# Performance work log

Measured on AMD Instinct MI355X. Metric: run time of the kernel, lower is better.

Reference implementation:

```python
import jax, jax.numpy as jnp
import numpy as np

A = 5          # angRes
C = 128        # channels
SPA = 2 * C    # spa_dim
NH = 8         # num_heads
KW = 11        # mask_field[1]


def setup_inputs() -> dict:
    key = jax.random.key(0)
    ks = jax.random.split(key, 12)
    s = 0.05
    return {
        "buffer": jax.random.normal(ks[0], (2, C, A * A, 32, 32), jnp.float32),
        "Win": jax.random.normal(ks[1], (SPA, C), jnp.float32) * s,
        "ln_w": jnp.ones((SPA,), jnp.float32),
        "ln_b": jnp.zeros((SPA,), jnp.float32),
        "in_proj": jax.random.normal(ks[2], (3 * SPA, SPA), jnp.float32) * s,
        "attn_out_w": jax.random.normal(ks[3], (SPA, SPA), jnp.float32) * s,
        "ffn_ln_w": jnp.ones((SPA,), jnp.float32),
        "ffn_ln_b": jnp.zeros((SPA,), jnp.float32),
        "ff1": jax.random.normal(ks[4], (2 * SPA, SPA), jnp.float32) * s,
        "ff2": jax.random.normal(ks[5], (SPA, 2 * SPA), jnp.float32) * s,
        "Wout": jax.random.normal(ks[6], (C, SPA), jnp.float32) * s,
        "conv_w": jax.random.normal(ks[7], (C, C, 1, 3, 3), jnp.float32) * s,
    }


def layer_norm(x, w, b, eps=1e-5):
    mu = x.mean(-1, keepdims=True)
    var = ((x - mu) ** 2).mean(-1, keepdims=True)
    return (x - mu) * jax.lax.rsqrt(var + eps) * w + b


def gen_mask(h, w, k_h, k_w):
    # additive mask over flattened (h*w) x (h*w) grid, local window k_h x k_w
    i = jnp.arange(h)
    j = jnp.arange(w)
    mh = (i[None, :] >= i[:, None] - k_h // 2) & (i[None, :] < i[:, None] + (k_h - k_h // 2))
    mw = (j[None, :] >= j[:, None] - k_w // 2) & (j[None, :] < j[:, None] + (k_w - k_w // 2))
    allowed = (mh[:, None, :, None] & mw[None, :, None, :]).reshape(h * w, h * w)
    return jnp.where(allowed, 0.0, -jnp.inf)


def basic_trans(x, Win, ln_w, ln_b, in_proj, attn_out_w,
                ffn_ln_w, ffn_ln_b, ff1, ff2, Wout):
    b, c, n, v, w = x.shape
    mask = gen_mask(v, w, 2 * A, KW)                       # (L, L)
    # 'b c n v w -> (v w) (b n) c'
    tok = x.transpose(3, 4, 0, 2, 1).reshape(v * w, b * n, c)
    tok = tok @ Win.T                                       # (L, B, E)
    tn = layer_norm(tok, ln_w, ln_b)
    L, B, E = tok.shape
    hd = E // NH
    Wq, Wk, Wv = jnp.split(in_proj, 3, axis=0)
    q = (tn @ Wq.T).reshape(L, B, NH, hd)
    k = (tn @ Wk.T).reshape(L, B, NH, hd)
    vv = (tok @ Wv.T).reshape(L, B, NH, hd)                 # value = un-normed tok
    scores = jnp.einsum('lbhd,mbhd->bhlm', q, k) / np.float32(np.sqrt(hd))
    scores = scores + mask[None, None]
    attn = jax.nn.softmax(scores, axis=-1)
    o = jnp.einsum('bhlm,mbhd->lbhd', attn, vv).reshape(L, B, E)
    tok = o @ attn_out_w.T + tok
    ff = layer_norm(tok, ffn_ln_w, ffn_ln_b)
    ff = jax.nn.relu(ff @ ff1.T) @ ff2.T
    tok = ff + tok
    tok = tok @ Wout.T                                      # (L, B, c)
    # '(v w) (b n) c -> b c n v w'
    return tok.reshape(v, w, b, n, c).transpose(2, 4, 3, 0, 1)


def reference(buffer, Win, ln_w, ln_b, in_proj, attn_out_w,
              ffn_ln_w, ffn_ln_b, ff1, ff2, Wout, conv_w):
    a = A
    b, c, uv, h, w = buffer.shape
    bt = lambda z: basic_trans(z, Win, ln_w, ln_b, in_proj, attn_out_w,
                               ffn_ln_w, ffn_ln_b, ff1, ff2, Wout)
    conv = lambda z: jax.lax.conv_general_dilated(
        z, conv_w, (1, 1, 1), ((0, 0), (1, 1), (1, 1)),
        dimension_numbers=('NCDHW', 'OIDHW', 'NCDHW'))

    # pass 1: 'b c (u v) h w -> b c (v w) u h'
    x = buffer.reshape(b, c, a, a, h, w).transpose(0, 1, 3, 5, 2, 4).reshape(b, c, a * w, a, h)
    x = bt(x)
    x = x.reshape(b, c, a, w, a, h).transpose(0, 1, 4, 2, 5, 3).reshape(b, c, a * a, h, w)
    x = conv(x) + buffer
    sc2 = x
    # pass 2: 'b c (u v) h w -> b c (u h) v w'
    y = x.reshape(b, c, a, a, h, w).transpose(0, 1, 2, 4, 3, 5).reshape(b, c, a * h, a, w)
    y = bt(y)
    y = y.reshape(b, c, a, h, a, w).transpose(0, 1, 2, 4, 3, 5).reshape(b, c, a * a, h, w)
    return conv(y) + sc2
```

## Files before the change

kernel.cpp:

```cpp
#include <hip/hip_runtime.h>
#include <math.h>
#include <stdint.h>

typedef __attribute__((ext_vector_type(8))) short bf16x8;
typedef __attribute__((ext_vector_type(4))) float f32x4;

static __device__ __forceinline__ unsigned short f2bf(float f) {
    unsigned u = __builtin_bit_cast(unsigned, f);
    unsigned r = u + 0x7fffu + ((u >> 16) & 1u);
    return (unsigned short)(r >> 16);
}
static __device__ __forceinline__ float bf2f(unsigned short h) {
    return __builtin_bit_cast(float, ((unsigned)h) << 16);
}
static __device__ __forceinline__ void gload_lds16(const void* g, void* l) {
    __builtin_amdgcn_global_load_lds((const __attribute__((address_space(1))) unsigned int*)g,
                                     (__attribute__((address_space(3))) unsigned int*)l, 16, 0, 0);
}

__global__ __launch_bounds__(256) void gather1(const float* __restrict__ src,
                                               unsigned short* __restrict__ x0, int W, int bb0) {
    int cct = blockIdx.x & 3, y = blockIdx.x >> 2;
    int n = blockIdx.y; int u = n / 5, v = n % 5;
    int lb = blockIdx.z, bb = bb0 + lb;
    __shared__ float tile[32][33];
    int tx = threadIdx.x & 31, tg = threadIdx.x >> 5;
    const float* s = src + (((size_t)(bb * 128 + cct * 32) * 25 + n) * 32 + y) * 32;
    #pragma unroll
    for (int i = 0; i < 4; i++) {
        int cl = tg + 8 * i;
        tile[cl][tx] = s[(size_t)cl * 25600 + tx];
    }
    __syncthreads();
    unsigned short* d = x0 + ((size_t)(u * 32 + y) * W + lb * 160 + v * 32) * 128 + cct * 32;
    #pragma unroll
    for (int i = 0; i < 4; i++) {
        int xx = tg + 8 * i;
        d[(size_t)xx * 128 + tx] = f2bf(tile[tx][xx]);
    }
}

__global__ __launch_bounds__(256) void gather2(const float* __restrict__ src,
                                               unsigned short* __restrict__ x0, int W, int bb0) {
    int cct = blockIdx.x & 3, x = blockIdx.x >> 2;
    int n = blockIdx.y; int u = n / 5, v = n % 5;
    int lb = blockIdx.z, bb = bb0 + lb;
    __shared__ float tile[32][33];
    int tx = threadIdx.x & 31, tg = threadIdx.x >> 5;
    const float* s = src + (((size_t)(bb * 128 + cct * 32) * 25 + n) * 32) * 32 + x;
    #pragma unroll
    for (int i = 0; i < 4; i++) {
        int cl = tg + 8 * i;
        tile[cl][tx] = s[(size_t)cl * 25600 + tx * 32];
    }
    __syncthreads();
    unsigned short* d = x0 + ((size_t)(v * 32 + x) * W + lb * 160 + u * 32) * 128 + cct * 32;
    #pragma unroll
    for (int i = 0; i < 4; i++) {
        int yy = tg + 8 * i;
        d[(size_t)yy * 128 + tx] = f2bf(tile[tx][yy]);
    }
}

__global__ __launch_bounds__(256) void repack_w(const float* __restrict__ cw,
                                                unsigned short* __restrict__ wb) {
    int g = blockIdx.x * 256 + threadIdx.x;
    int co = g / 1152;
    int rem = g - co * 1152;
    int ci = rem / 9, tap = rem - ci * 9;
    wb[((size_t)tap * 128 + co) * 128 + ci] = f2bf(cw[g]);
}

__global__ __launch_bounds__(256) void conv_weights(const float* __restrict__ Win,
                                                    const float* __restrict__ in_proj,
                                                    const float* __restrict__ attn_out_w,
                                                    const float* __restrict__ ff1,
                                                    const float* __restrict__ ff2,
                                                    const float* __restrict__ Wout,
                                                    unsigned short* __restrict__ wg) {
    int g = blockIdx.x * 256 + threadIdx.x;
    float v;
    if      (g < 32768)  v = Win[g];
    else if (g < 229376) v = in_proj[g - 32768];
    else if (g < 294912) v = attn_out_w[g - 229376];
    else if (g < 425984) v = ff1[g - 294912];
    else if (g < 557056) v = ff2[g - 425984];
    else                 v = Wout[g - 557056];
    wg[g] = f2bf(v);
}

__global__ __launch_bounds__(256) void ln_bf16(const unsigned short* __restrict__ in,
                                               unsigned short* __restrict__ out,
                                               const float* __restrict__ w, const float* __restrict__ b) {
    int tok = blockIdx.x * 4 + (threadIdx.x >> 6);
    int lane = threadIdx.x & 63;
    ushort4 h4 = ((const ushort4*)(in + (size_t)tok * 256))[lane];
    float vx = bf2f(h4.x), vy = bf2f(h4.y), vz = bf2f(h4.z), vw = bf2f(h4.w);
    float s = vx + vy + vz + vw;
    #pragma unroll
    for (int off = 32; off > 0; off >>= 1) s += __shfl_xor(s, off);
    float mu = s * (1.0f / 256.0f);
    float dx = vx - mu, dy = vy - mu, dz = vz - mu, dw = vw - mu;
    float vs = dx * dx + dy * dy + dz * dz + dw * dw;
    #pragma unroll
    for (int off = 32; off > 0; off >>= 1) vs += __shfl_xor(vs, off);
    float inv = rsqrtf(vs * (1.0f / 256.0f) + 1e-5f);
    float4 wv = ((const float4*)w)[lane];
    float4 bv = ((const float4*)b)[lane];
    ushort4 o4;
    o4.x = f2bf(dx * inv * wv.x + bv.x);
    o4.y = f2bf(dy * inv * wv.y + bv.y);
    o4.z = f2bf(dz * inv * wv.z + bv.z);
    o4.w = f2bf(dw * inv * wv.w + bv.w);
    *(ushort4*)(out + (size_t)tok * 256 + lane * 4) = o4;
}

static __device__ __forceinline__ void xcd_remap(int& bxi, int& byi) {
    int d = blockIdx.x + gridDim.x * blockIdx.y;
    int s = d & 7;
    unsigned j = (unsigned)(d >> 3);
    unsigned ny = gridDim.y;
    int gm8 = (int)(gridDim.x >> 3);
    bxi = s * gm8 + (int)(j / ny);
    byi = (int)(j % ny);
}

static __device__ __forceinline__ void gemm_core64(const unsigned short* __restrict__ X,
                                                   const unsigned short* __restrict__ Wt,
                                                   int bm, int bnrow, int K,
                                                   unsigned short (&As)[2][64 * 32],
                                                   unsigned short (&Bs)[2][64 * 32],
                                                   f32x4 (&acc)[2][2]) {
    const int tid = threadIdx.x;
    const int lane = tid & 63, w = tid >> 6;
    const int wm = (w >> 1) * 32, wn = (w & 1) * 32;
    const int lr = lane & 15, lq = lane >> 4;
    #pragma unroll
    for (int m = 0; m < 2; m++)
        #pragma unroll
        for (int n = 0; n < 2; n++)
            acc[m][n] = (f32x4){0.f, 0.f, 0.f, 0.f};

    const int srow = tid >> 2, sslot = tid & 3;
    const int ssl = sslot ^ ((srow >> 1) & 3);
    auto STAGE = [&](int bsel, int k0) {
        gload_lds16(X  + (size_t)(bm + srow) * K + k0 + ssl * 8,
                    &As[bsel][tid * 8]);
        gload_lds16(Wt + (size_t)(bnrow + srow) * K + k0 + ssl * 8,
                    &Bs[bsel][tid * 8]);
    };

    const int nt = K >> 5;
    STAGE(0, 0);
    __syncthreads();
    int cur = 0;
    for (int t = 0; t < nt; ++t) {
        if (t + 1 < nt) STAGE(cur ^ 1, (t + 1) << 5);
        const char* Ab = (const char*)As[cur];
        const char* Bb = (const char*)Bs[cur];
        bf16x8 af[2], bf[2];
        #pragma unroll
        for (int m = 0; m < 2; m++) {
            int row = wm + m * 16 + lr;
            af[m] = *(const bf16x8*)(Ab + row * 64 + ((lq * 16) ^ (((row >> 1) & 3) << 4)));
        }
        #pragma unroll
        for (int n = 0; n < 2; n++) {
            int row = wn + n * 16 + lr;
            bf[n] = *(const bf16x8*)(Bb + row * 64 + ((lq * 16) ^ (((row >> 1) & 3) << 4)));
        }
        #pragma unroll
        for (int m = 0; m < 2; m++)
            #pragma unroll
            for (int n = 0; n < 2; n++)
                acc[m][n] = __builtin_amdgcn_mfma_f32_16x16x32_bf16(af[m], bf[n], acc[m][n], 0, 0, 0);
        if (t + 1 < nt) __syncthreads();
        cur ^= 1;
    }
}

__global__ __launch_bounds__(256) void gemm_bf16(const unsigned short* __restrict__ X,
                                                 const unsigned short* __restrict__ Wt,
                                                 unsigned short* __restrict__ Yb,
                                                 const unsigned short* __restrict__ Rb,
                                                 int N, int K, int relu, int spass, int W) {
    __shared__ unsigned short As[2][64 * 32];
    __shared__ unsigned short Bs[2][64 * 32];
    int bxi, byi;
    xcd_remap(bxi, byi);
    const int bm = bxi * 64, bn = byi * 64;
    f32x4 acc[2][2];
    gemm_core64(X, Wt, bm, bn, K, As, Bs, acc);

    const int lane = threadIdx.x & 63, w = threadIdx.x >> 6;
    const int wm = (w >> 1) * 32, wn = (w & 1) * 32;
    const int lr = lane & 15, lq = lane >> 4;
    #pragma unroll
    for (int m = 0; m < 2; m++) {
        #pragma unroll
        for (int r = 0; r < 4; r++) {
            int row = bm + wm + m * 16 + lq * 4 + r;
            size_t base;
            if (spass == 0) {
                base = (size_t)row * N;
            } else {
                int l = row / W, c = row - l * W;
                int lb = (c >= 160) ? 1 : 0, sp = c - lb * 160;
                int sl_, pix;
                if (spass == 1) { int u = l >> 5, y = l & 31, v = sp >> 5, x = sp & 31;
                                  sl_ = lb * 25 + u * 5 + v; pix = y * 32 + x; }
                else            { int v = l >> 5, x = l & 31, u = sp >> 5, y = sp & 31;
                                  sl_ = lb * 25 + u * 5 + v; pix = y * 32 + x; }
                base = ((size_t)sl_ * 1024 + pix) * 128;
            }
            #pragma unroll
            for (int n = 0; n < 2; n++) {
                int col = bn + wn + n * 16 + lr;
                float val = acc[m][n][r];
                if (Rb) val += bf2f(Rb[(size_t)row * N + col]);
                if (relu) val = fmaxf(val, 0.0f);
                Yb[base + col] = f2bf(val);
            }
        }
    }
}

__global__ __launch_bounds__(256) void gemm_qkv(const unsigned short* __restrict__ tn,
                                                const unsigned short* __restrict__ tok,
                                                const unsigned short* __restrict__ Wqkv,
                                                unsigned short* __restrict__ QK,
                                                unsigned short* __restrict__ V) {
    __shared__ unsigned short As[2][64 * 32];
    __shared__ unsigned short Bs[2][64 * 32];
    int bxi, by;
    xcd_remap(bxi, by);
    const int bm = bxi * 64;
    const unsigned short* X = (by < 8) ? tn : tok;
    f32x4 acc[2][2];
    gemm_core64(X, Wqkv, bm, by * 64, 256, As, Bs, acc);

    unsigned short* Yb = (by < 8) ? QK : V;
    const int N = (by < 8) ? 512 : 256;
    const int bn = (by < 8) ? by * 64 : (by - 8) * 64;
    const int lane = threadIdx.x & 63, w = threadIdx.x >> 6;
    const int wm = (w >> 1) * 32, wn = (w & 1) * 32;
    const int lr = lane & 15, lq = lane >> 4;
    #pragma unroll
    for (int m = 0; m < 2; m++) {
        #pragma unroll
        for (int r = 0; r < 4; r++) {
            int row = bm + wm + m * 16 + lq * 4 + r;
            #pragma unroll
            for (int n = 0; n < 2; n++) {
                int col = bn + wn + n * 16 + lr;
                Yb[(size_t)row * N + col] = f2bf(acc[m][n][r]);
            }
        }
    }
}

__global__ __launch_bounds__(256) void ffn_fused(const unsigned short* __restrict__ X,
                                                 const unsigned short* __restrict__ W1,
                                                 const unsigned short* __restrict__ W2,
                                                 unsigned short* __restrict__ R) {
    __shared__ unsigned short Wc[64 * 256];
    __shared__ unsigned short Hs[64 * 64];
    const int tid = threadIdx.x;
    const int lane = tid & 63, w = tid >> 6;
    const int lr = lane & 15, lq = lane >> 4;
    const int thm = (w >> 1) * 32;
    const int thb = (w & 1) * 32;
    const int hh  = (w >> 1) * 32;
    const int wn2 = (w & 1) * 128;
    const int bm = blockIdx.x * 64;

    bf16x8 xf[2][8];
    #pragma unroll
    for (int nt = 0; nt < 2; nt++) {
        const unsigned short* xr = X + (size_t)(bm + thb + nt * 16 + lr) * 256 + lq * 8;
        #pragma unroll
        for (int ks = 0; ks < 8; ks++)
            xf[nt][ks] = *(const bf16x8*)(xr + ks * 32);
    }

    f32x4 acc_o[2][8];
    #pragma unroll
    for (int m = 0; m < 2; m++)
        #pragma unroll
        for (int nt = 0; nt < 8; nt++)
            acc_o[m][nt] = (f32x4){0.f, 0.f, 0.f, 0.f};

    for (int hk = 0; hk < 8; hk++) {
        if (hk) __syncthreads();
        #pragma unroll
        for (int i = 0; i < 8; i++) {
            int d = (w << 13) + (i << 10) + (lane << 4);
            int h = d >> 9, s = (d >> 4) & 31;
            int ss = s ^ (h & 7);
            gload_lds16(W1 + (size_t)(hk * 64 + h) * 256 + ss * 8,
                        (char*)Wc + (w << 13) + (i << 10));
        }
        __syncthreads();

        f32x4 acc1[2][2];
        #pragma unroll
        for (int mh = 0; mh < 2; mh++)
            #pragma unroll
            for (int nt = 0; nt < 2; nt++)
                acc1[mh][nt] = (f32x4){0.f, 0.f, 0.f, 0.f};
        #pragma unroll
        for (int ks = 0; ks < 8; ks++) {
            bf16x8 w1f[2];
            #pragma unroll
            for (int mh = 0; mh < 2; mh++) {
                int hrow = hh + mh * 16 + lr;
                int slot = ks * 4 + lq;
                w1f[mh] = *(const bf16x8*)((const char*)Wc + hrow * 512 + ((slot ^ (hrow & 7)) << 4));
            }
            #pragma unroll
            for (int mh = 0; mh < 2; mh++)
                #pragma unroll
                for (int nt = 0; nt < 2; nt++)
                    acc1[mh][nt] = __builtin_amdgcn_mfma_f32_16x16x32_bf16(w1f[mh], xf[nt][ks], acc1[mh][nt], 0, 0, 0);
        }
        #pragma unroll
        for (int mh = 0; mh < 2; mh++)
            #pragma unroll
            for (int nt = 0; nt < 2; nt++) {
                int hid0 = hh + mh * 16 + lq * 4;
                int tokr = thb + nt * 16 + lr;
                ushort4 pk;
                pk.x = f2bf(fmaxf(acc1[mh][nt][0], 0.0f));
                pk.y = f2bf(fmaxf(acc1[mh][nt][1], 0.0f));
                pk.z = f2bf(fmaxf(acc1[mh][nt][2], 0.0f));
                pk.w = f2bf(fmaxf(acc1[mh][nt][3], 0.0f));
                *(ushort4*)((char*)Hs + tokr * 128 +
                            (((hid0 >> 3) ^ (tokr & 7)) << 4) + (hid0 & 7) * 2) = pk;
            }
        __syncthreads();

        #pragma unroll
        for (int i = 0; i < 8; i++) {
            int d = (w << 13) + (i << 10) + (lane << 4);
            int o = d >> 7, s = (d >> 4) & 7;
            int ss = s ^ (o & 7);
            gload_lds16(W2 + (size_t)o * 512 + hk * 64 + ss * 8,
                        (char*)Wc + (w << 13) + (i << 10));
        }
        __syncthreads();

        #pragma unroll
        for (int ks = 0; ks < 2; ks++) {
            int slot = ks * 4 + lq;
            bf16x8 af2[2];
            #pragma unroll
            for (int m = 0; m < 2; m++) {
                int trow = thm + m * 16 + lr;
                af2[m] = *(const bf16x8*)((const char*)Hs + trow * 128 + ((slot ^ (trow & 7)) << 4));
            }
            #pragma unroll
            for (int nt = 0; nt < 8; nt++) {
                int orow = wn2 + nt * 16 + lr;
                bf16x8 b2 = *(const bf16x8*)((const char*)Wc + orow * 128 + ((slot ^ (orow & 7)) << 4));
                #pragma unroll
                for (int m = 0; m < 2; m++)
                    acc_o[m][nt] = __builtin_amdgcn_mfma_f32_16x16x32_bf16(af2[m], b2, acc_o[m][nt], 0, 0, 0);
            }
        }
    }
    #pragma unroll
    for (int m = 0; m < 2; m++)
        #pragma unroll
        for (int nt = 0; nt < 8; nt++)
            #pragma unroll
            for (int r = 0; r < 4; r++) {
                int row = bm + thm + m * 16 + lq * 4 + r;
                int col = wn2 + nt * 16 + lr;
                size_t off = (size_t)row * 256 + col;
                R[off] = f2bf(acc_o[m][nt][r] + bf2f(R[off]));
            }
}

__global__ __launch_bounds__(256) void vtrans(const unsigned short* __restrict__ vtok,
                                              unsigned short* __restrict__ vt, int W) {
    const int col = blockIdx.x, h = blockIdx.y;
    __shared__ unsigned short t[160][34];
    const int tid = threadIdx.x;
    for (int i = tid; i < 160 * 16; i += 256) {
        int l = i >> 4, dp = i & 15;
        unsigned v = *(const unsigned*)(vtok + ((size_t)l * W + col) * 256 + h * 32 + dp * 2);
        *(unsigned*)&t[l][dp * 2] = v;
    }
    __syncthreads();
    unsigned short* dst = vt + (((size_t)h * W + col) * 32) * 160;
    for (int i = tid; i < 32 * 160; i += 256) {
        int d = i / 160, l = i - d * 160;
        dst[i] = t[l][d];
    }
}

__global__ __launch_bounds__(64) void attn_mfma(const unsigned short* __restrict__ qk,
                                                const unsigned short* __restrict__ vt,
                                                unsigned short* __restrict__ o, int W) {
    const int col = blockIdx.x;
    const int h = blockIdx.y;
    const int lane = threadIdx.x;
    const int lr = lane & 15, lq = lane >> 4;
    __shared__ __align__(16) unsigned short P_lds[16][168];

    bf16x8 kf[10];
    #pragma unroll
    for (int m = 0; m < 10; m++) {
        size_t t = (size_t)(m * 16 + lr) * W + col;
        kf[m] = *(const bf16x8*)(qk + t * 512 + 256 + h * 32 + lq * 8);
    }
    const unsigned short* vbase = vt + (((size_t)h * W + col) * 32) * 160;
    bf16x8 vf[2][5];
    #pragma unroll
    for (int md = 0; md < 2; md++)
        #pragma unroll
        for (int c = 0; c < 5; c++)
            vf[md][c] = *(const bf16x8*)(vbase + (size_t)(md * 16 + lr) * 160 + c * 32 + lq * 8);

    const float scale = 0.17677669529663687f;
    for (int n = 0; n < 10; n++) {
        const int q = n * 16 + lr;
        bf16x8 qf = *(const bf16x8*)(qk + ((size_t)q * W + col) * 512 + h * 32 + lq * 8);
        f32x4 p[10];
        #pragma unroll
        for (int m = 0; m < 10; m++)
            p[m] = __builtin_amdgcn_mfma_f32_16x16x32_bf16(kf[m], qf, (f32x4){0.f,0.f,0.f,0.f}, 0, 0, 0);
        const int b = lq * 4 - ((n & 1) * 16 + lr);
        float mx = -1e30f;
        #pragma unroll
        for (int m = 0; m < 10; m++) {
            #pragma unroll
            for (int r = 0; r < 4; r++) {
                int dd = b + (m & 1) * 16 + r;
                float s = ((unsigned)(dd + 5) <= 10u) ? p[m][r] : -1e30f;
                p[m][r] = s;
                mx = fmaxf(mx, s);
            }
        }
        mx = fmaxf(mx, __shfl_xor(mx, 16));
        mx = fmaxf(mx, __shfl_xor(mx, 32));
        float sum = 0.f;
        #pragma unroll
        for (int m = 0; m < 10; m++) {
            #pragma unroll
            for (int r = 0; r < 4; r++) {
                float e = __expf((p[m][r] - mx) * scale);
                p[m][r] = e;
                sum += e;
            }
        }
        sum += __shfl_xor(sum, 16);
        sum += __shfl_xor(sum, 32);
        #pragma unroll
        for (int m = 0; m < 10; m++) {
            ushort4 pk;
            pk.x = f2bf(p[m][0]); pk.y = f2bf(p[m][1]);
            pk.z = f2bf(p[m][2]); pk.w = f2bf(p[m][3]);
            *(ushort4*)&P_lds[lr][m * 16 + lq * 4] = pk;
        }
        f32x4 oa0 = (f32x4){0.f,0.f,0.f,0.f}, oa1 = (f32x4){0.f,0.f,0.f,0.f};
        #pragma unroll
        for (int c = 0; c < 5; c++) {
            bf16x8 pf = *(const bf16x8*)&P_lds[lr][c * 32 + lq * 8];
            oa0 = __builtin_amdgcn_mfma_f32_16x16x32_bf16(vf[0][c], pf, oa0, 0, 0, 0);
            oa1 = __builtin_amdgcn_mfma_f32_16x16x32_bf16(vf[1][c], pf, oa1, 0, 0, 0);
        }
        const float inv = 1.0f / sum;
        unsigned short* op = o + ((size_t)q * W + col) * 256 + h * 32;
        ushort4 s0, s1;
        s0.x = f2bf(oa0[0] * inv); s0.y = f2bf(oa0[1] * inv);
        s0.z = f2bf(oa0[2] * inv); s0.w = f2bf(oa0[3] * inv);
        s1.x = f2bf(oa1[0] * inv); s1.y = f2bf(oa1[1] * inv);
        s1.z = f2bf(oa1[2] * inv); s1.w = f2bf(oa1[3] * inv);
        *(ushort4*)(op + lq * 4)      = s0;
        *(ushort4*)(op + 16 + lq * 4) = s1;
    }
}

__global__ __launch_bounds__(256) void conv_mfma(const unsigned short* __restrict__ xp,
                                                 const unsigned short* __restrict__ wb,
                                                 const float* __restrict__ res,
                                                 float* __restrict__ out, int bb0) {
    const int ptile = blockIdx.x;
    const int slice = blockIdx.y;
    const int lb = slice / 25, n = slice % 25;
    const int bb = bb0 + lb;
    const int y0 = ptile * 4;
    __shared__ unsigned short As[128 * 64];
    __shared__ unsigned short Bs[128 * 64];
    const int tid = threadIdx.x;
    const int lane = tid & 63, w = tid >> 6;
    const int wm = (w >> 1) * 64;
    const int wn = (w & 1) * 64;
    const int lr = lane & 15, lq = lane >> 4;
    const unsigned short* xs = xp + (size_t)slice * 1024 * 128;
    f32x4 acc[4][4];
    #pragma unroll
    for (int m = 0; m < 4; m++)
        #pragma unroll
        for (int nn = 0; nn < 4; nn++)
            acc[m][nn] = (f32x4){0.f, 0.f, 0.f, 0.f};

    for (int tap = 0; tap < 9; tap++) {
        const int dy = tap / 3 - 1, dx = tap % 3 - 1;
        for (int c0 = 0; c0 < 128; c0 += 64) {
            #pragma unroll
            for (int i = 0; i < 4; i++) {
                int id = tid + 256 * i;
                int row = id >> 3, cg = id & 7;
                int py = y0 + (row >> 5) + dy;
                int px = (row & 31) + dx;
                uint4 v = {0u, 0u, 0u, 0u};
                if ((unsigned)py < 32u && (unsigned)px < 32u)
                    v = *(const uint4*)(xs + ((size_t)(py * 32 + px) * 128 + c0 + cg * 8));
                int boff = row * 128 + ((cg * 16) ^ ((row & 7) << 4));
                *(uint4*)((char*)As + boff) = v;
            }
            #pragma unroll
            for (int i = 0; i < 4; i++) {
                int id = tid + 256 * i;
                int row = id >> 3, cg = id & 7;
                uint4 v = *(const uint4*)(wb + (((size_t)tap * 128 + row) * 128 + c0 + cg * 8));
                int boff = row * 128 + ((cg * 16) ^ ((row & 7) << 4));
                *(uint4*)((char*)Bs + boff) = v;
            }
            __syncthreads();
            #pragma unroll
            for (int ks = 0; ks < 2; ks++) {
                bf16x8 wf[4], xf[4];
                #pragma unroll
                for (int m = 0; m < 4; m++) {
                    int row = wm + m * 16 + lr;
                    int boff = row * 128 + ((ks * 64 + lq * 16) ^ ((row & 7) << 4));
                    wf[m] = *(const bf16x8*)((const char*)Bs + boff);
                }
                #pragma unroll
                for (int nn = 0; nn < 4; nn++) {
                    int row = wn + nn * 16 + lr;
                    int boff = row * 128 + ((ks * 64 + lq * 16) ^ ((row & 7) << 4));
                    xf[nn] = *(const bf16x8*)((const char*)As + boff);
                }
                #pragma unroll
                for (int m = 0; m < 4; m++)
                    #pragma unroll
                    for (int nn = 0; nn < 4; nn++)
                        acc[m][nn] = __builtin_amdgcn_mfma_f32_16x16x32_bf16(wf[m], xf[nn], acc[m][nn], 0, 0, 0);
            }
            __syncthreads();
        }
    }
    #pragma unroll
    for (int m = 0; m < 4; m++) {
        int co0 = wm + m * 16 + lq * 4;
        #pragma unroll
        for (int r = 0; r < 4; r++) {
            size_t rowoff = (((size_t)(bb * 128 + co0 + r) * 25 + n) * 1024) + ptile * 128;
            #pragma unroll
            for (int nn = 0; nn < 4; nn++) {
                int pix = wn + nn * 16 + lr;
                out[rowoff + pix] = acc[m][nn][r] + res[rowoff + pix];
            }
        }
    }
}

extern "C" void kernel_launch(void* const* d_in, const int* in_sizes, int n_in,
                              void* d_out, int out_size, void* d_ws, size_t ws_size,
                              hipStream_t stream) {
    (void)in_sizes; (void)n_in; (void)out_size;
    const float* buffer     = (const float*)d_in[0];
    const float* Win        = (const float*)d_in[1];
    const float* ln_w       = (const float*)d_in[2];
    const float* ln_b       = (const float*)d_in[3];
    const float* in_proj    = (const float*)d_in[4];
    const float* attn_out_w = (const float*)d_in[5];
    const float* ffn_ln_w   = (const float*)d_in[6];
    const float* ffn_ln_b   = (const float*)d_in[7];
    const float* ff1        = (const float*)d_in[8];
    const float* ff2        = (const float*)d_in[9];
    const float* Wout       = (const float*)d_in[10];
    const float* conv_w     = (const float*)d_in[11];
    float* out = (float*)d_out;
    float* ws  = (float*)d_ws;

    const size_t need2 = ((size_t)51200 * 960 + 368640) * 4;
    int NBB = (ws_size >= need2) ? 2 : 1;
    const int W = NBB * 160;
    const size_t T = (size_t)NBB * 25600;

    unsigned short* x0b   = (unsigned short*)ws;
    unsigned short* Abf   = (unsigned short*)(ws + T * 64);
    unsigned short* tnb   = (unsigned short*)(ws + T * 192);
    float*          C     = ws + T * 320;
    unsigned short* QKtok = (unsigned short*)C;
    unsigned short* Vtok  = (unsigned short*)(C + T * 256);
    unsigned short* Vt    = (unsigned short*)(C + T * 384);
    unsigned short* xp    = (unsigned short*)C;
    unsigned short* Db    = (unsigned short*)(ws + T * 832);
    unsigned short* wg    = (unsigned short*)(ws + T * 960);
    unsigned short* wb    = (unsigned short*)(ws + T * 960 + 294912);

    const unsigned short* Winb  = wg;
    const unsigned short* Wqkvb = wg + 32768;
    const unsigned short* Waob  = wg + 229376;
    const unsigned short* Wff1b = wg + 294912;
    const unsigned short* Wff2b = wg + 425984;
    const unsigned short* Woutb = wg + 557056;

    const int GM64 = (int)(T / 64);

    conv_weights<<<2304, 256, 0, stream>>>(Win, in_proj, attn_out_w, ff1, ff2, Wout, wg);
    repack_w<<<576, 256, 0, stream>>>(conv_w, wb);

    for (int pass = 0; pass < 2; pass++) {
        const float* src = (pass == 0) ? buffer : out;
        for (int bb0 = 0; bb0 < 2; bb0 += NBB) {
            if (pass == 0) gather1<<<dim3(128, 25, NBB), 256, 0, stream>>>(src, x0b, W, bb0);
            else           gather2<<<dim3(128, 25, NBB), 256, 0, stream>>>(src, x0b, W, bb0);

            gemm_bf16<<<dim3(GM64, 4), 256, 0, stream>>>(x0b, Winb, Abf, nullptr, 256, 128, 0, 0, W);
            ln_bf16<<<(int)(T / 4), 256, 0, stream>>>(Abf, tnb, ln_w, ln_b);
            gemm_qkv<<<dim3(GM64, 12), 256, 0, stream>>>(tnb, Abf, Wqkvb, QKtok, Vtok);
            vtrans<<<dim3(W, 8), 256, 0, stream>>>(Vtok, Vt, W);
            attn_mfma<<<dim3(W, 8), 64, 0, stream>>>(QKtok, Vt, Db, W);
            gemm_bf16<<<dim3(GM64, 4), 256, 0, stream>>>(Db, Waob, Abf, Abf, 256, 256, 0, 0, W);
            ln_bf16<<<(int)(T / 4), 256, 0, stream>>>(Abf, tnb, ffn_ln_w, ffn_ln_b);
            ffn_fused<<<GM64, 256, 0, stream>>>(tnb, Wff1b, Wff2b, Abf);
            gemm_bf16<<<dim3(GM64, 2), 256, 0, stream>>>(Abf, Woutb, xp, nullptr, 128, 256, 0, pass + 1, W);

            conv_mfma<<<dim3(8, NBB * 25), 256, 0, stream>>>(
                xp, wb, (pass == 0) ? buffer : (const float*)out, out, bb0);
        }
    }
}
```

Baseline: 560.4 us.

## Load FFN weights and activations directly from global memory instead of LDS staging

The fused FFN kernel no longer stages W1 and W2 tiles into shared memory through async global-to-LDS copies. MFMA operands for both GEMMs are now read straight from global memory, relying on L1/L2 caching, and the X fragments are reloaded per k-step instead of held in registers. This removes the 32KB LDS buffer and two barriers per iteration, which should cut LDS footprint and register pressure and raise occupancy. In exchange each wave issues many redundant uncoalesced global loads with no staging to hide their latency.

New measurement: 721.6 us. 28.8% more time.

```diff
diff --git a/kernel.cpp b/kernel.cpp
--- a/kernel.cpp
+++ b/kernel.cpp
@@ -263,7 +263,6 @@
                                                  const unsigned short* __restrict__ W1,
                                                  const unsigned short* __restrict__ W2,
                                                  unsigned short* __restrict__ R) {
-    __shared__ unsigned short Wc[64 * 256];
     __shared__ unsigned short Hs[64 * 64];
     const int tid = threadIdx.x;
     const int lane = tid & 63, w = tid >> 6;
@@ -274,15 +273,6 @@
     const int wn2 = (w & 1) * 128;
     const int bm = blockIdx.x * 64;
 
-    bf16x8 xf[2][8];
-    #pragma unroll
-    for (int nt = 0; nt < 2; nt++) {
-        const unsigned short* xr = X + (size_t)(bm + thb + nt * 16 + lr) * 256 + lq * 8;
-        #pragma unroll
-        for (int ks = 0; ks < 8; ks++)
-            xf[nt][ks] = *(const bf16x8*)(xr + ks * 32);
-    }
-
     f32x4 acc_o[2][8];
     #pragma unroll
     for (int m = 0; m < 2; m++)
@@ -291,17 +281,6 @@
             acc_o[m][nt] = (f32x4){0.f, 0.f, 0.f, 0.f};
 
     for (int hk = 0; hk < 8; hk++) {
-        if (hk) __syncthreads();
-        #pragma unroll
-        for (int i = 0; i < 8; i++) {
-            int d = (w << 13) + (i << 10) + (lane << 4);
-            int h = d >> 9, s = (d >> 4) & 31;
-            int ss = s ^ (h & 7);
-            gload_lds16(W1 + (size_t)(hk * 64 + h) * 256 + ss * 8,
-                        (char*)Wc + (w << 13) + (i << 10));
-        }
-        __syncthreads();
-
         f32x4 acc1[2][2];
         #pragma unroll
         for (int mh = 0; mh < 2; mh++)
@@ -310,19 +289,20 @@
                 acc1[mh][nt] = (f32x4){0.f, 0.f, 0.f, 0.f};
         #pragma unroll
         for (int ks = 0; ks < 8; ks++) {
-            bf16x8 w1f[2];
-            #pragma unroll
-            for (int mh = 0; mh < 2; mh++) {
-                int hrow = hh + mh * 16 + lr;
-                int slot = ks * 4 + lq;
-                w1f[mh] = *(const bf16x8*)((const char*)Wc + hrow * 512 + ((slot ^ (hrow & 7)) << 4));
-            }
+            bf16x8 w1f[2], xtf[2];
+            #pragma unroll
+            for (int mh = 0; mh < 2; mh++)
+                w1f[mh] = *(const bf16x8*)(W1 + (size_t)(hk * 64 + hh + mh * 16 + lr) * 256 + ks * 32 + lq * 8);
+            #pragma unroll
+            for (int nt = 0; nt < 2; nt++)
+                xtf[nt] = *(const bf16x8*)(X + (size_t)(bm + thb + nt * 16 + lr) * 256 + ks * 32 + lq * 8);
             #pragma unroll
             for (int mh = 0; mh < 2; mh++)
                 #pragma unroll
                 for (int nt = 0; nt < 2; nt++)
-                    acc1[mh][nt] = __builtin_amdgcn_mfma_f32_16x16x32_bf16(w1f[mh], xf[nt][ks], acc1[mh][nt], 0, 0, 0);
-        }
+                    acc1[mh][nt] = __builtin_amdgcn_mfma_f32_16x16x32_bf16(w1f[mh], xtf[nt], acc1[mh][nt], 0, 0, 0);
+        }
+        if (hk) __syncthreads();
         #pragma unroll
         for (int mh = 0; mh < 2; mh++)
             #pragma unroll
@@ -340,16 +320,6 @@
         __syncthreads();
 
         #pragma unroll
-        for (int i = 0; i < 8; i++) {
-            int d = (w << 13) + (i << 10) + (lane << 4);
-            int o = d >> 7, s = (d >> 4) & 7;
-            int ss = s ^ (o & 7);
-            gload_lds16(W2 + (size_t)o * 512 + hk * 64 + ss * 8,
-                        (char*)Wc + (w << 13) + (i << 10));
-        }
-        __syncthreads();
-
-        #pragma unroll
         for (int ks = 0; ks < 2; ks++) {
             int slot = ks * 4 + lq;
             bf16x8 af2[2];
@@ -360,8 +330,7 @@
             }
             #pragma unroll
             for (int nt = 0; nt < 8; nt++) {
-                int orow = wn2 + nt * 16 + lr;
-                bf16x8 b2 = *(const bf16x8*)((const char*)Wc + orow * 128 + ((slot ^ (orow & 7)) << 4));
+                bf16x8 b2 = *(const bf16x8*)(W2 + (size_t)(wn2 + nt * 16 + lr) * 512 + hk * 64 + ks * 32 + lq * 8);
                 #pragma unroll
                 for (int m = 0; m < 2; m++)
                     acc_o[m][nt] = __builtin_amdgcn_mfma_f32_16x16x32_bf16(af2[m], b2, acc_o[m][nt], 0, 0, 0);
```

## Fuse LayerNorm into full-row GEMM epilogue for input and attention-out projections

Applied to the files above, without the earlier changes.

Adds a gemm_ln kernel where each block computes a full 64x256 output tile, optionally adds the residual, then computes the per-row mean and variance using shuffles plus a small LDS reduction. It writes both the raw bf16 output and the normalized output. This removes the separate ln_bf16 launches and their re-read of the intermediate. In exchange the grid has 4x fewer blocks, each with more accumulator registers and LDS. Variance is now computed as E[x^2]-mu^2, which is less numerically stable.

Result: no change. 557.1 us (-0.6%).

```diff
diff --git a/kernel.cpp b/kernel.cpp
--- a/kernel.cpp
+++ b/kernel.cpp
@@ -89,32 +89,6 @@
     wg[g] = f2bf(v);
 }
 
-__global__ __launch_bounds__(256) void ln_bf16(const unsigned short* __restrict__ in,
-                                               unsigned short* __restrict__ out,
-                                               const float* __restrict__ w, const float* __restrict__ b) {
-    int tok = blockIdx.x * 4 + (threadIdx.x >> 6);
-    int lane = threadIdx.x & 63;
-    ushort4 h4 = ((const ushort4*)(in + (size_t)tok * 256))[lane];
-    float vx = bf2f(h4.x), vy = bf2f(h4.y), vz = bf2f(h4.z), vw = bf2f(h4.w);
-    float s = vx + vy + vz + vw;
-    #pragma unroll
-    for (int off = 32; off > 0; off >>= 1) s += __shfl_xor(s, off);
-    float mu = s * (1.0f / 256.0f);
-    float dx = vx - mu, dy = vy - mu, dz = vz - mu, dw = vw - mu;
-    float vs = dx * dx + dy * dy + dz * dz + dw * dw;
-    #pragma unroll
-    for (int off = 32; off > 0; off >>= 1) vs += __shfl_xor(vs, off);
-    float inv = rsqrtf(vs * (1.0f / 256.0f) + 1e-5f);
-    float4 wv = ((const float4*)w)[lane];
-    float4 bv = ((const float4*)b)[lane];
-    ushort4 o4;
-    o4.x = f2bf(dx * inv * wv.x + bv.x);
-    o4.y = f2bf(dy * inv * wv.y + bv.y);
-    o4.z = f2bf(dz * inv * wv.z + bv.z);
-    o4.w = f2bf(dw * inv * wv.w + bv.w);
-    *(ushort4*)(out + (size_t)tok * 256 + lane * 4) = o4;
-}
-
 static __device__ __forceinline__ void xcd_remap(int& bxi, int& byi) {
     int d = blockIdx.x + gridDim.x * blockIdx.y;
     int s = d & 7;
@@ -257,6 +231,131 @@
             }
         }
     }
+}
+
+__global__ __launch_bounds__(256) void gemm_ln(const unsigned short* __restrict__ X,
+                                               const unsigned short* __restrict__ Wt,
+                                               const unsigned short* __restrict__ Rb,
+                                               unsigned short* __restrict__ Yraw,
+                                               unsigned short* __restrict__ Tn,
+                                               const float* __restrict__ lnw,
+                                               const float* __restrict__ lnb, int K) {
+    __shared__ unsigned short As[2][64 * 32];
+    __shared__ unsigned short Bs[2][256 * 32];
+    __shared__ float red_s[64][2], red_q[64][2];
+    const int tid = threadIdx.x;
+    const int lane = tid & 63, w = tid >> 6;
+    const int lr = lane & 15, lq = lane >> 4;
+    const int thm = (w >> 1) * 32;
+    const int wn2 = (w & 1) * 128;
+    const int bm = blockIdx.x * 64;
+
+    f32x4 acc[2][8];
+    #pragma unroll
+    for (int m = 0; m < 2; m++)
+        #pragma unroll
+        for (int n = 0; n < 8; n++)
+            acc[m][n] = (f32x4){0.f, 0.f, 0.f, 0.f};
+
+    const int srow = tid >> 2, sslot = tid & 3;
+    auto STAGE = [&](int bsel, int k0) {
+        {   int ssl = sslot ^ ((srow >> 1) & 3);
+            gload_lds16(X + (size_t)(bm + srow) * K + k0 + ssl * 8, &As[bsel][tid * 8]); }
+        #pragma unroll
+        for (int i = 0; i < 4; i++) {
+            int row = i * 64 + srow;
+            int ssl = sslot ^ ((row >> 1) & 3);
+            gload_lds16(Wt + (size_t)row * K + k0 + ssl * 8, &Bs[bsel][(i * 256 + tid) * 8]);
+        }
+    };
+
+    const int ntk = K >> 5;
+    STAGE(0, 0);
+    __syncthreads();
+    int cur = 0;
+    for (int t = 0; t < ntk; ++t) {
+        if (t + 1 < ntk) STAGE(cur ^ 1, (t + 1) << 5);
+        const char* Ab = (const char*)As[cur];
+        const char* Bb = (const char*)Bs[cur];
+        bf16x8 af[2], bf[8];
+        #pragma unroll
+        for (int m = 0; m < 2; m++) {
+            int row = thm + m * 16 + lr;
+            af[m] = *(const bf16x8*)(Ab + row * 64 + ((lq * 16) ^ (((row >> 1) & 3) << 4)));
+        }
+        #pragma unroll
+        for (int n = 0; n < 8; n++) {
+            int row = wn2 + n * 16 + lr;
+            bf[n] = *(const bf16x8*)(Bb + row * 64 + ((lq * 16) ^ (((row >> 1) & 3) << 4)));
+        }
+        #pragma unroll
+        for (int m = 0; m < 2; m++)
+            #pragma unroll
+            for (int n = 0; n < 8; n++)
+                acc[m][n] = __builtin_amdgcn_mfma_f32_16x16x32_bf16(af[m], bf[n], acc[m][n], 0, 0, 0);
+        if (t + 1 < ntk) __syncthreads();
+        cur ^= 1;
+    }
+
+    if (Rb) {
+        #pragma unroll
+        for (int m = 0; m < 2; m++)
+            #pragma unroll
+            for (int n = 0; n < 8; n++)
+                #pragma unroll
+                for (int r = 0; r < 4; r++) {
+                    int row = bm + thm + m * 16 + lq * 4 + r;
+                    int col = wn2 + n * 16 + lr;
+                    acc[m][n][r] += bf2f(Rb[(size_t)row * 256 + col]);
+                }
+    }
+    #pragma unroll
+    for (int m = 0; m < 2; m++)
+        #pragma unroll
+        for (int r = 0; r < 4; r++) {
+            float s = 0.f, q = 0.f;
+            #pragma unroll
+            for (int n = 0; n < 8; n++) {
+                float v = acc[m][n][r];
+                s += v; q += v * v;
+            }
+            #pragma unroll
+            for (int off = 1; off < 16; off <<= 1) {
+                s += __shfl_xor(s, off);
+                q += __shfl_xor(q, off);
+            }
+            if (lr == 0) {
+                int rt = thm + m * 16 + lq * 4 + r;
+                red_s[rt][w & 1] = s;
+                red_q[rt][w & 1] = q;
+            }
+        }
+    __syncthreads();
+    float wv[8], bv[8];
+    #pragma unroll
+    for (int n = 0; n < 8; n++) {
+        wv[n] = lnw[wn2 + n * 16 + lr];
+        bv[n] = lnb[wn2 + n * 16 + lr];
+    }
+    #pragma unroll
+    for (int m = 0; m < 2; m++)
+        #pragma unroll
+        for (int r = 0; r < 4; r++) {
+            int rt = thm + m * 16 + lq * 4 + r;
+            float s = red_s[rt][0] + red_s[rt][1];
+            float q = red_q[rt][0] + red_q[rt][1];
+            float mu = s * (1.0f / 256.0f);
+            float inv = rsqrtf(q * (1.0f / 256.0f) - mu * mu + 1e-5f);
+            int row = bm + rt;
+            #pragma unroll
+            for (int n = 0; n < 8; n++) {
+                int col = wn2 + n * 16 + lr;
+                float v = acc[m][n][r];
+                size_t off = (size_t)row * 256 + col;
+                Yraw[off] = f2bf(v);
+                Tn[off]   = f2bf((v - mu) * inv * wv[n] + bv[n]);
+            }
+        }
 }
 
 __global__ __launch_bounds__(256) void ffn_fused(const unsigned short* __restrict__ X,
@@ -623,13 +722,11 @@
             if (pass == 0) gather1<<<dim3(128, 25, NBB), 256, 0, stream>>>(src, x0b, W, bb0);
             else           gather2<<<dim3(128, 25, NBB), 256, 0, stream>>>(src, x0b, W, bb0);
 
-            gemm_bf16<<<dim3(GM64, 4), 256, 0, stream>>>(x0b, Winb, Abf, nullptr, 256, 128, 0, 0, W);
-            ln_bf16<<<(int)(T / 4), 256, 0, stream>>>(Abf, tnb, ln_w, ln_b);
+            gemm_ln<<<GM64, 256, 0, stream>>>(x0b, Winb, nullptr, Abf, tnb, ln_w, ln_b, 128);
             gemm_qkv<<<dim3(GM64, 12), 256, 0, stream>>>(tnb, Abf, Wqkvb, QKtok, Vtok);
             vtrans<<<dim3(W, 8), 256, 0, stream>>>(Vtok, Vt, W);
             attn_mfma<<<dim3(W, 8), 64, 0, stream>>>(QKtok, Vt, Db, W);
-            gemm_bf16<<<dim3(GM64, 4), 256, 0, stream>>>(Db, Waob, Abf, Abf, 256, 256, 0, 0, W);
-            ln_bf16<<<(int)(T / 4), 256, 0, stream>>>(Abf, tnb, ffn_ln_w, ffn_ln_b);
+            gemm_ln<<<GM64, 256, 0, stream>>>(Db, Waob, Abf, Abf, tnb, ffn_ln_w, ffn_ln_b, 256);
             ffn_fused<<<GM64, 256, 0, stream>>>(tnb, Wff1b, Wff2b, Abf);
             gemm_bf16<<<dim3(GM64, 2), 256, 0, stream>>>(Abf, Woutb, xp, nullptr, 128, 256, 0, pass + 1, W);
 
```
